# Kernel optimization log

Measured on AMD Instinct MI355X. Metric: run time of the kernel, lower is better.

The kernel has to match this reference:

```python
import jax, jax.numpy as jnp
import numpy as np

N, C, B = 131072, 256, 2
Z, Y, X = 32, 240, 240  # spconv coord order: batch, z, y, x
EPS = 1e-5


def _build_sparse():
    """Generate unique sparse voxel coords and per-axis 3-tap submanifold
    neighbor tables (rulebook). Sentinel index N marks a missing neighbor."""
    rng = np.random.default_rng(0)
    per = N // B
    coords = []
    for b in range(B):
        lin = rng.choice(Z * Y * X, per, replace=False)
        z, r = np.divmod(lin, Y * X)
        y, x = np.divmod(r, X)
        coords.append(np.stack([np.full(per, b), z, y, x], 1))
    coords = np.concatenate(coords, 0).astype(np.int64)
    keys = ((coords[:, 0] * Z + coords[:, 1]) * Y + coords[:, 2]) * X + coords[:, 3]
    order = np.argsort(keys)
    coords, keys = coords[order], keys[order]

    def nbr_axis(axis, bound):
        out = np.full((N, 3), N, dtype=np.int64)
        for k, off in enumerate((-1, 0, 1)):
            c = coords.copy()
            c[:, axis] += off
            valid = (c[:, axis] >= 0) & (c[:, axis] < bound)
            qk = ((c[:, 0] * Z + c[:, 1]) * Y + c[:, 2]) * X + c[:, 3]
            pos = np.clip(np.searchsorted(keys, qk), 0, N - 1)
            hit = valid & (keys[pos] == qk)
            out[:, k] = np.where(hit, pos, N)
        return out

    return nbr_axis(1, Z), nbr_axis(2, Y), nbr_axis(3, X)


def setup_inputs() -> dict:
    nbr1, nbr2, nbr3 = _build_sparse()
    key = jax.random.key(0)
    ks = jax.random.split(key, 4)
    scale = 0.02  # keep pre-sigmoid activations in a sane range
    return {
        "features": jax.random.normal(ks[0], (N, C), jnp.float32),
        "W1": jax.random.normal(ks[1], (3, C, C), jnp.float32) * scale,
        "W2": jax.random.normal(ks[2], (3, C, C), jnp.float32) * scale,
        "W3": jax.random.normal(ks[3], (3, C, C), jnp.float32) * scale,
        "g1": jnp.ones((C,), jnp.float32), "b1": jnp.zeros((C,), jnp.float32),
        "g2": jnp.ones((C,), jnp.float32), "b2": jnp.zeros((C,), jnp.float32),
        "g3": jnp.ones((C,), jnp.float32), "b3": jnp.zeros((C,), jnp.float32),
        "nbr1": jnp.asarray(nbr1), "nbr2": jnp.asarray(nbr2), "nbr3": jnp.asarray(nbr3),
    }


def _subm_conv(fp, nbr, W):
    # fp: [N+1, C] (last row zero pad), nbr: [N, 3], W: [3, Cin, Cout]
    return fp[nbr[:, 0]] @ W[0] + fp[nbr[:, 1]] @ W[1] + fp[nbr[:, 2]] @ W[2]


def _bn(h, g, b):
    mu = h.mean(0)
    var = h.var(0)  # biased, matches torch BN normalization in train mode
    return g * (h - mu) * jax.lax.rsqrt(var + EPS) + b


def reference(features, W1, W2, W3, g1, b1, g2, b2, g3, b3, nbr1, nbr2, nbr3):
    pad = jnp.zeros((1, features.shape[1]), features.dtype)
    fp = jnp.concatenate([features, pad], 0)  # [N+1, C]
    s1 = jax.nn.sigmoid(_bn(_subm_conv(fp, nbr1, W1), g1, b1))
    s2 = jax.nn.sigmoid(_bn(_subm_conv(fp, nbr2, W2), g2, b2))
    s3 = jax.nn.sigmoid(_bn(_subm_conv(fp, nbr3, W3), g3, b3))
    return (s1 + s2 + s3) * features
```

## Files before the change

kernel.cpp:

```cpp
#include <hip/hip_runtime.h>
#include <hip/hip_bf16.h>


#define NP 131072
#define CC 256

typedef __attribute__((ext_vector_type(4))) float f32x4;
typedef __attribute__((ext_vector_type(8))) short bf16x8;

__device__ __forceinline__ unsigned short f2bf(float f) {
    unsigned int u = __float_as_uint(f);
    u += 0x7FFFu + ((u >> 16) & 1u);
    return (unsigned short)(u >> 16);
}
__device__ __forceinline__ float bf2f(unsigned short s) {
    return __uint_as_float(((unsigned int)s) << 16);
}

__device__ __forceinline__ void gload_lds16(const void* g, void* l) {
    __builtin_amdgcn_global_load_lds(
        (const __attribute__((address_space(1))) unsigned int*)g,
        (__attribute__((address_space(3))) unsigned int*)l, 16, 0, 0);
}

__global__ void zero_stats_k(float* stats) {
    int i = blockIdx.x * 256 + threadIdx.x;
    if (i < 3 * 2 * CC) stats[i] = 0.f;
}

__global__ void cast_features_k(const float* __restrict__ f, unsigned short* __restrict__ fb) {
    size_t e = ((size_t)blockIdx.x * 256 + threadIdx.x) * 8;
    const size_t tot = (size_t)(NP + 1) * CC;
    if (e >= tot) return;
    unsigned short tmp[8];
    if (e >= (size_t)NP * CC) {
        #pragma unroll
        for (int j = 0; j < 8; ++j) tmp[j] = 0;
    } else {
        float4 v0 = *(const float4*)(f + e);
        float4 v1 = *(const float4*)(f + e + 4);
        tmp[0] = f2bf(v0.x); tmp[1] = f2bf(v0.y); tmp[2] = f2bf(v0.z); tmp[3] = f2bf(v0.w);
        tmp[4] = f2bf(v1.x); tmp[5] = f2bf(v1.y); tmp[6] = f2bf(v1.z); tmp[7] = f2bf(v1.w);
    }
    *(bf16x8*)(fb + e) = *(bf16x8*)tmp;
}

__global__ void cast_weights_k(const float* __restrict__ W1, const float* __restrict__ W2,
                               const float* __restrict__ W3, unsigned short* __restrict__ wbT) {
    int bid  = blockIdx.x;
    int m    = bid >> 8;
    int cout = bid & 255;
    int cin  = threadIdx.x;
    const float* W = (m < 3) ? W1 : (m < 6) ? W2 : W3;
    int tap = m - (m / 3) * 3;
    float v = W[((size_t)tap * CC + cin) * CC + cout];
    wbT[((size_t)m * CC + cout) * CC + cin] = f2bf(v);
}

__global__ __launch_bounds__(256)
void gemm_conv_fused_k(const unsigned short* __restrict__ fb,
                       const unsigned short* __restrict__ wbT,
                       const int* __restrict__ nbr1, const int* __restrict__ nbr2,
                       const int* __restrict__ nbr3,
                       unsigned short* __restrict__ hbase,
                       float* __restrict__ statsBase) {
    __shared__ unsigned short As[128 * 32];
    __shared__ unsigned short Bs[128 * 32];
    __shared__ int rowIdx[3 * 128];
    __shared__ float colsum[128];
    __shared__ float colsq[128];

    const int axis = blockIdx.z;
    const int* nbr = (axis == 0) ? nbr1 : (axis == 1) ? nbr2 : nbr3;
    const unsigned short* wT = wbT + (size_t)axis * 3 * CC * CC;
    unsigned short* h = hbase + (size_t)axis * NP * CC;
    float* stats = statsBase + axis * 2 * CC;

    const int tid     = threadIdx.x;
    const int lane    = tid & 63;
    const int wave    = tid >> 6;
    const int colBase = blockIdx.x * 128;
    const int rowBase = blockIdx.y * 128;

    if (tid < 128) {
        int i = rowBase + tid;
        rowIdx[tid]       = nbr[(size_t)i * 3 + 0];
        rowIdx[128 + tid] = nbr[(size_t)i * 3 + 1];
        rowIdx[256 + tid] = nbr[(size_t)i * 3 + 2];
        colsum[tid] = 0.f;
        colsq[tid]  = 0.f;
    }

    f32x4 acc[4][4] = {};

    const int wr     = wave >> 1;
    const int wc     = wave & 1;
    const int fr     = lane & 15;
    const int sSub   = lane >> 2;
    const int sChunk = lane & 3;
    const int gChunk = sChunk ^ ((sSub >> 1) & 3);
    const int rChunkOff = ((lane >> 4) ^ ((fr >> 1) & 3)) * 8;

    __syncthreads();

    for (int tap = 0; tap < 3; ++tap) {
        const unsigned short* wTt = wT + (size_t)tap * CC * CC;
        const int* rIdx = rowIdx + tap * 128;
        for (int kk = 0; kk < CC; kk += 32) {
            #pragma unroll
            for (int u = 0; u < 2; ++u) {
                int q  = wave * 2 + u;
                int ar = rIdx[q * 16 + sSub];
                const unsigned short* asrc = fb + ((size_t)ar * CC + kk + gChunk * 8);
                gload_lds16(asrc, As + q * 512);
                int bc = colBase + q * 16 + sSub;
                const unsigned short* bsrc = wTt + ((size_t)bc * CC + kk + gChunk * 8);
                gload_lds16(bsrc, Bs + q * 512);
            }
            __syncthreads();

            bf16x8 aF[4], bF[4];
            #pragma unroll
            for (int m = 0; m < 4; ++m)
                aF[m] = *(const bf16x8*)(As + (wr * 64 + m * 16 + fr) * 32 + rChunkOff);
            #pragma unroll
            for (int n = 0; n < 4; ++n)
                bF[n] = *(const bf16x8*)(Bs + (wc * 64 + n * 16 + fr) * 32 + rChunkOff);
            #pragma unroll
            for (int m = 0; m < 4; ++m)
                #pragma unroll
                for (int n = 0; n < 4; ++n)
                    acc[m][n] = __builtin_amdgcn_mfma_f32_16x16x32_bf16(aF[m], bF[n], acc[m][n], 0, 0, 0);
            __syncthreads();
        }
    }

    const int orow = (lane >> 4) * 4;
    float psum[4], psq[4];
    #pragma unroll
    for (int n = 0; n < 4; ++n) { psum[n] = 0.f; psq[n] = 0.f; }
    #pragma unroll
    for (int m = 0; m < 4; ++m) {
        #pragma unroll
        for (int n = 0; n < 4; ++n) {
            int col = colBase + wc * 64 + n * 16 + fr;
            int row = rowBase + wr * 64 + m * 16 + orow;
            #pragma unroll
            for (int j = 0; j < 4; ++j) {
                unsigned short hb = f2bf(acc[m][n][j]);
                float v = bf2f(hb);
                h[(size_t)(row + j) * CC + col] = hb;
                psum[n] += v;
                psq[n]  += v * v;
            }
        }
    }
    #pragma unroll
    for (int n = 0; n < 4; ++n) {
        psum[n] += __shfl_xor(psum[n], 16);
        psum[n] += __shfl_xor(psum[n], 32);
        psq[n]  += __shfl_xor(psq[n], 16);
        psq[n]  += __shfl_xor(psq[n], 32);
    }
    if ((lane >> 4) == 0) {
        #pragma unroll
        for (int n = 0; n < 4; ++n) {
            int cl = wc * 64 + n * 16 + fr;
            atomicAdd(&colsum[cl], psum[n]);
            atomicAdd(&colsq[cl],  psq[n]);
        }
    }
    __syncthreads();
    if (tid < 128) {
        int c = colBase + tid;
        atomicAdd(&stats[c],      colsum[tid]);
        atomicAdd(&stats[CC + c], colsq[tid]);
    }
}

__global__ void finalize3_k(const float* __restrict__ stats,
                            const float* __restrict__ g1, const float* __restrict__ b1,
                            const float* __restrict__ g2, const float* __restrict__ b2,
                            const float* __restrict__ g3, const float* __restrict__ b3,
                            float* __restrict__ ss) {
    int a = blockIdx.x;
    int c = threadIdx.x;
    const float* g = (a == 0) ? g1 : (a == 1) ? g2 : g3;
    const float* b = (a == 0) ? b1 : (a == 1) ? b2 : b3;
    const float* st = stats + a * 2 * CC;
    float* s = ss + a * 2 * CC;
    float mu  = st[c] * (1.f / NP);
    float var = st[CC + c] * (1.f / NP) - mu * mu;
    float sc  = g[c] * rsqrtf(var + 1e-5f);
    s[c]      = sc;
    s[CC + c] = b[c] - mu * sc;
}

__global__ void apply3_k(const unsigned short* __restrict__ h1,
                         const unsigned short* __restrict__ h2,
                         const unsigned short* __restrict__ h3,
                         const float* __restrict__ ss,
                         const float* __restrict__ feat, float* __restrict__ out) {
    size_t e = ((size_t)blockIdx.x * 256 + threadIdx.x) * 8;
    int c0 = (int)(e & (CC - 1));
    bf16x8 v1 = *(const bf16x8*)(h1 + e);
    bf16x8 v2 = *(const bf16x8*)(h2 + e);
    bf16x8 v3 = *(const bf16x8*)(h3 + e);
    float s[8];
    #pragma unroll
    for (int j = 0; j < 8; ++j) {
        float z1 = ss[c0 + j]            * bf2f((unsigned short)v1[j]) + ss[CC + c0 + j];
        float z2 = ss[2 * CC + c0 + j]   * bf2f((unsigned short)v2[j]) + ss[3 * CC + c0 + j];
        float z3 = ss[4 * CC + c0 + j]   * bf2f((unsigned short)v3[j]) + ss[5 * CC + c0 + j];
        s[j] = 1.f / (1.f + __expf(-z1)) + 1.f / (1.f + __expf(-z2)) + 1.f / (1.f + __expf(-z3));
    }
    const float4* fv = (const float4*)(feat + e);
    float4 f0 = fv[0], f1 = fv[1];
    float4* o = (float4*)(out + e);
    o[0] = make_float4(s[0] * f0.x, s[1] * f0.y, s[2] * f0.z, s[3] * f0.w);
    o[1] = make_float4(s[4] * f1.x, s[5] * f1.y, s[6] * f1.z, s[7] * f1.w);
}

extern "C" void kernel_launch(void* const* d_in, const int* in_sizes, int n_in,
                              void* d_out, int out_size, void* d_ws, size_t ws_size,
                              hipStream_t stream) {
    const float* feat = (const float*)d_in[0];
    const float* W1   = (const float*)d_in[1];
    const float* W2   = (const float*)d_in[2];
    const float* W3   = (const float*)d_in[3];
    const float* g1   = (const float*)d_in[4];
    const float* b1   = (const float*)d_in[5];
    const float* g2   = (const float*)d_in[6];
    const float* b2   = (const float*)d_in[7];
    const float* g3   = (const float*)d_in[8];
    const float* b3   = (const float*)d_in[9];
    const int* nbr1   = (const int*)d_in[10];
    const int* nbr2   = (const int*)d_in[11];
    const int* nbr3   = (const int*)d_in[12];
    float* out = (float*)d_out;

    char* w = (char*)d_ws;
    unsigned short* fb   = (unsigned short*)w;  w += (size_t)(NP + 1) * CC * 2;
    unsigned short* wbT  = (unsigned short*)w;  w += (size_t)9 * CC * CC * 2;
    float* stats         = (float*)w;           w += (size_t)3 * 2 * CC * 4;
    float* ss            = (float*)w;           w += (size_t)3 * 2 * CC * 4;
    unsigned short* hbuf = (unsigned short*)w;

    zero_stats_k<<<6, 256, 0, stream>>>(stats);
    {
        size_t tot = (size_t)(NP + 1) * CC / 8;
        int blocks = (int)((tot + 255) / 256);
        cast_features_k<<<blocks, 256, 0, stream>>>(feat, fb);
    }
    cast_weights_k<<<2304, 256, 0, stream>>>(W1, W2, W3, wbT);

    gemm_conv_fused_k<<<dim3(2, 1024, 3), 256, 0, stream>>>(fb, wbT, nbr1, nbr2, nbr3,
                                                            hbuf, stats);
    finalize3_k<<<3, 256, 0, stream>>>(stats, g1, b1, g2, b2, g3, b3, ss);
    apply3_k<<<16384, 256, 0, stream>>>(hbuf,
                                        hbuf + (size_t)NP * CC,
                                        hbuf + (size_t)2 * NP * CC,
                                        ss, feat, out);
}
```

Baseline: 321.8 us.

## Rewrite gathered conv GEMM with 256x256 tiles and double-buffered LDS pipeline

The conv GEMM is restructured so each 512-thread block computes a 256-row by full 256-column tile with BK=64. LDS is double-buffered, and the async global-to-LDS loads for the next k-step are interleaved with MFMA phases, using setprio and barriers to overlap memory and compute. Each gathered feature row is now read once instead of once per column half, which cuts gather traffic. The epilogue and apply kernel use nontemporal loads and stores, and the apply kernel reads bf16 features instead of fp32. That last change introduces rounding error in the final multiply by the features.

```diff
diff --git a/kernel.cpp b/kernel.cpp
--- a/kernel.cpp
+++ b/kernel.cpp
@@ -4,6 +4,10 @@
 
 #define NP 131072
 #define CC 256
+#define BM 256
+#define BK 64
+#define ATILE (BM * BK)
+#define BTILE (256 * BK)
 
 typedef __attribute__((ext_vector_type(4))) float f32x4;
 typedef __attribute__((ext_vector_type(8))) short bf16x8;
@@ -57,82 +61,155 @@
     wbT[((size_t)m * CC + cout) * CC + cin] = f2bf(v);
 }
 
-__global__ __launch_bounds__(256)
+#define MFMA16(a, b, c) __builtin_amdgcn_mfma_f32_16x16x32_bf16((a), (b), (c), 0, 0, 0)
+#define LDF(base, row, swz) (*(const bf16x8*)((base) + (row) * BK + (swz)))
+
+__global__ __launch_bounds__(512, 2)
 void gemm_conv_fused_k(const unsigned short* __restrict__ fb,
                        const unsigned short* __restrict__ wbT,
                        const int* __restrict__ nbr1, const int* __restrict__ nbr2,
                        const int* __restrict__ nbr3,
                        unsigned short* __restrict__ hbase,
                        float* __restrict__ statsBase) {
-    __shared__ unsigned short As[128 * 32];
-    __shared__ unsigned short Bs[128 * 32];
-    __shared__ int rowIdx[3 * 128];
-    __shared__ float colsum[128];
-    __shared__ float colsq[128];
-
-    const int axis = blockIdx.z;
+    __shared__ unsigned short As[2 * ATILE];
+    __shared__ unsigned short Bs[2 * BTILE];
+    __shared__ float colsum[256];
+    __shared__ float colsq[256];
+
+    const int axis = blockIdx.y;
     const int* nbr = (axis == 0) ? nbr1 : (axis == 1) ? nbr2 : nbr3;
-    const unsigned short* wT = wbT + (size_t)axis * 3 * CC * CC;
+    const unsigned short* wA = wbT + (size_t)axis * 3 * CC * CC;
     unsigned short* h = hbase + (size_t)axis * NP * CC;
     float* stats = statsBase + axis * 2 * CC;
 
     const int tid     = threadIdx.x;
     const int lane    = tid & 63;
     const int wave    = tid >> 6;
-    const int colBase = blockIdx.x * 128;
-    const int rowBase = blockIdx.y * 128;
-
-    if (tid < 128) {
-        int i = rowBase + tid;
-        rowIdx[tid]       = nbr[(size_t)i * 3 + 0];
-        rowIdx[128 + tid] = nbr[(size_t)i * 3 + 1];
-        rowIdx[256 + tid] = nbr[(size_t)i * 3 + 2];
-        colsum[tid] = 0.f;
-        colsq[tid]  = 0.f;
-    }
-
-    f32x4 acc[4][4] = {};
-
-    const int wr     = wave >> 1;
-    const int wc     = wave & 1;
-    const int fr     = lane & 15;
-    const int sSub   = lane >> 2;
-    const int sChunk = lane & 3;
-    const int gChunk = sChunk ^ ((sSub >> 1) & 3);
-    const int rChunkOff = ((lane >> 4) ^ ((fr >> 1) & 3)) * 8;
-
+    const int rowBase = blockIdx.x * BM;
+
+    if (tid < 256) { colsum[tid] = 0.f; colsq[tid] = 0.f; }
+
+    int rstage[4], srcOff[4];
+    int gA0[4], gA1[4], gA2[4];
+    #pragma unroll
+    for (int u = 0; u < 4; ++u) {
+        int idx = u * 512 + tid;
+        int r = idx >> 3, p = idx & 7;
+        rstage[u] = r;
+        srcOff[u] = (p ^ (r & 7)) * 8;
+        int gi = rowBase + r;
+        gA0[u] = nbr[(size_t)gi * 3 + 0];
+        gA1[u] = nbr[(size_t)gi * 3 + 1];
+        gA2[u] = nbr[(size_t)gi * 3 + 2];
+    }
+
+#define STAGE_A(u, Abuf, tapsel, kkE) do {                                    \
+        int gr_ = ((tapsel) == 0) ? gA0[u] : ((tapsel) == 1) ? gA1[u] : gA2[u]; \
+        gload_lds16(fb + (size_t)gr_ * CC + (kkE) + srcOff[u],                \
+                    (Abuf) + ((u) * 512 + wave * 64) * 8);                    \
+    } while (0)
+#define STAGE_B(u, Bbuf, wTt, kkE)                                            \
+        gload_lds16((wTt) + (size_t)rstage[u] * CC + (kkE) + srcOff[u],       \
+                    (Bbuf) + ((u) * 512 + wave * 64) * 8)
+
+    const int wr = wave >> 2;
+    const int wc = wave & 3;
+    const int fr = lane & 15;
+    const int kq = lane >> 4;
+    const int swz0 = (kq ^ (fr & 7)) * 8;
+    const int swz1 = ((4 + kq) ^ (fr & 7)) * 8;
+    const int rA = wr * 128 + fr;
+    const int rB = wc * 64 + fr;
+
+    f32x4 acc[8][4] = {};
+
+    STAGE_A(0, As, 0, 0); STAGE_A(1, As, 0, 0); STAGE_A(2, As, 0, 0); STAGE_A(3, As, 0, 0);
+    STAGE_B(0, Bs, wA, 0); STAGE_B(1, Bs, wA, 0); STAGE_B(2, Bs, wA, 0); STAGE_B(3, Bs, wA, 0);
     __syncthreads();
 
-    for (int tap = 0; tap < 3; ++tap) {
-        const unsigned short* wTt = wT + (size_t)tap * CC * CC;
-        const int* rIdx = rowIdx + tap * 128;
-        for (int kk = 0; kk < CC; kk += 32) {
-            #pragma unroll
-            for (int u = 0; u < 2; ++u) {
-                int q  = wave * 2 + u;
-                int ar = rIdx[q * 16 + sSub];
-                const unsigned short* asrc = fb + ((size_t)ar * CC + kk + gChunk * 8);
-                gload_lds16(asrc, As + q * 512);
-                int bc = colBase + q * 16 + sSub;
-                const unsigned short* bsrc = wTt + ((size_t)bc * CC + kk + gChunk * 8);
-                gload_lds16(bsrc, Bs + q * 512);
-            }
-            __syncthreads();
-
-            bf16x8 aF[4], bF[4];
-            #pragma unroll
-            for (int m = 0; m < 4; ++m)
-                aF[m] = *(const bf16x8*)(As + (wr * 64 + m * 16 + fr) * 32 + rChunkOff);
-            #pragma unroll
-            for (int n = 0; n < 4; ++n)
-                bF[n] = *(const bf16x8*)(Bs + (wc * 64 + n * 16 + fr) * 32 + rChunkOff);
-            #pragma unroll
-            for (int m = 0; m < 4; ++m)
-                #pragma unroll
-                for (int n = 0; n < 4; ++n)
-                    acc[m][n] = __builtin_amdgcn_mfma_f32_16x16x32_bf16(aF[m], bF[n], acc[m][n], 0, 0, 0);
-            __syncthreads();
-        }
+    for (int t = 0; t < 12; ++t) {
+        unsigned short* Ac = As + (t & 1) * ATILE;
+        unsigned short* Bc = Bs + (t & 1) * BTILE;
+        unsigned short* An = As + ((t & 1) ^ 1) * ATILE;
+        unsigned short* Bn = Bs + ((t & 1) ^ 1) * BTILE;
+        const int t1 = t + 1;
+        const int tap1 = t1 >> 2;
+        const int kk1 = (t1 & 3) * BK;
+        const unsigned short* wT1 = wA + (size_t)tap1 * CC * CC;
+        const bool st = (t < 11);
+
+        bf16x8 aF[4][2], bLo[2][2], bHi[2][2];
+
+        #pragma unroll
+        for (int m = 0; m < 4; ++m) {
+            aF[m][0] = LDF(Ac, rA + m * 16, swz0);
+            aF[m][1] = LDF(Ac, rA + m * 16, swz1);
+        }
+        #pragma unroll
+        for (int n = 0; n < 2; ++n) {
+            bLo[n][0] = LDF(Bc, rB + n * 16, swz0);
+            bLo[n][1] = LDF(Bc, rB + n * 16, swz1);
+        }
+        if (st) { STAGE_A(0, An, tap1, kk1); STAGE_A(1, An, tap1, kk1); STAGE_B(0, Bn, wT1, kk1); }
+        __builtin_amdgcn_s_barrier();
+        __builtin_amdgcn_s_setprio(1);
+        #pragma unroll
+        for (int m = 0; m < 4; ++m)
+            #pragma unroll
+            for (int n = 0; n < 2; ++n) {
+                acc[m][n] = MFMA16(aF[m][0], bLo[n][0], acc[m][n]);
+                acc[m][n] = MFMA16(aF[m][1], bLo[n][1], acc[m][n]);
+            }
+        __builtin_amdgcn_s_setprio(0);
+        __builtin_amdgcn_s_barrier();
+
+        #pragma unroll
+        for (int n = 0; n < 2; ++n) {
+            bHi[n][0] = LDF(Bc, rB + (n + 2) * 16, swz0);
+            bHi[n][1] = LDF(Bc, rB + (n + 2) * 16, swz1);
+        }
+        if (st) { STAGE_A(2, An, tap1, kk1); STAGE_A(3, An, tap1, kk1); STAGE_B(1, Bn, wT1, kk1); }
+        __builtin_amdgcn_s_barrier();
+        __builtin_amdgcn_s_setprio(1);
+        #pragma unroll
+        for (int m = 0; m < 4; ++m)
+            #pragma unroll
+            for (int n = 0; n < 2; ++n) {
+                acc[m][n + 2] = MFMA16(aF[m][0], bHi[n][0], acc[m][n + 2]);
+                acc[m][n + 2] = MFMA16(aF[m][1], bHi[n][1], acc[m][n + 2]);
+            }
+        __builtin_amdgcn_s_setprio(0);
+        __builtin_amdgcn_s_barrier();
+
+        #pragma unroll
+        for (int m = 0; m < 4; ++m) {
+            aF[m][0] = LDF(Ac, rA + (m + 4) * 16, swz0);
+            aF[m][1] = LDF(Ac, rA + (m + 4) * 16, swz1);
+        }
+        if (st) { STAGE_B(2, Bn, wT1, kk1); STAGE_B(3, Bn, wT1, kk1); }
+        __builtin_amdgcn_s_barrier();
+        __builtin_amdgcn_s_setprio(1);
+        #pragma unroll
+        for (int m = 0; m < 4; ++m)
+            #pragma unroll
+            for (int n = 0; n < 2; ++n) {
+                acc[m + 4][n + 2] = MFMA16(aF[m][0], bHi[n][0], acc[m + 4][n + 2]);
+                acc[m + 4][n + 2] = MFMA16(aF[m][1], bHi[n][1], acc[m + 4][n + 2]);
+            }
+        __builtin_amdgcn_s_setprio(0);
+        __builtin_amdgcn_s_barrier();
+
+        __builtin_amdgcn_s_setprio(1);
+        #pragma unroll
+        for (int m = 0; m < 4; ++m)
+            #pragma unroll
+            for (int n = 0; n < 2; ++n) {
+                acc[m + 4][n] = MFMA16(aF[m][0], bLo[n][0], acc[m + 4][n]);
+                acc[m + 4][n] = MFMA16(aF[m][1], bLo[n][1], acc[m + 4][n]);
+            }
+        __builtin_amdgcn_s_setprio(0);
+        if (st) asm volatile("s_waitcnt vmcnt(0)" ::: "memory");
+        __builtin_amdgcn_s_barrier();
     }
 
     const int orow = (lane >> 4) * 4;
@@ -140,16 +217,16 @@
     #pragma unroll
     for (int n = 0; n < 4; ++n) { psum[n] = 0.f; psq[n] = 0.f; }
     #pragma unroll
-    for (int m = 0; m < 4; ++m) {
+    for (int m = 0; m < 8; ++m) {
         #pragma unroll
         for (int n = 0; n < 4; ++n) {
-            int col = colBase + wc * 64 + n * 16 + fr;
-            int row = rowBase + wr * 64 + m * 16 + orow;
+            int col = wc * 64 + n * 16 + fr;
+            int row = rowBase + wr * 128 + m * 16 + orow;
             #pragma unroll
             for (int j = 0; j < 4; ++j) {
                 unsigned short hb = f2bf(acc[m][n][j]);
                 float v = bf2f(hb);
-                h[(size_t)(row + j) * CC + col] = hb;
+                __builtin_nontemporal_store(hb, &h[(size_t)(row + j) * CC + col]);
                 psum[n] += v;
                 psq[n]  += v * v;
             }
@@ -171,11 +248,12 @@
         }
     }
     __syncthreads();
-    if (tid < 128) {
-        int c = colBase + tid;
-        atomicAdd(&stats[c],      colsum[tid]);
-        atomicAdd(&stats[CC + c], colsq[tid]);
-    }
+    if (tid < 256) {
+        atomicAdd(&stats[tid],      colsum[tid]);
+        atomicAdd(&stats[CC + tid], colsq[tid]);
+    }
+#undef STAGE_A
+#undef STAGE_B
 }
 
 __global__ void finalize3_k(const float* __restrict__ stats,
@@ -200,25 +278,27 @@
                          const unsigned short* __restrict__ h2,
                          const unsigned short* __restrict__ h3,
                          const float* __restrict__ ss,
-                         const float* __restrict__ feat, float* __restrict__ out) {
+                         const unsigned short* __restrict__ fb, float* __restrict__ out) {
     size_t e = ((size_t)blockIdx.x * 256 + threadIdx.x) * 8;
     int c0 = (int)(e & (CC - 1));
-    bf16x8 v1 = *(const bf16x8*)(h1 + e);
-    bf16x8 v2 = *(const bf16x8*)(h2 + e);
-    bf16x8 v3 = *(const bf16x8*)(h3 + e);
+    bf16x8 v1 = __builtin_nontemporal_load((const bf16x8*)(h1 + e));
+    bf16x8 v2 = __builtin_nontemporal_load((const bf16x8*)(h2 + e));
+    bf16x8 v3 = __builtin_nontemporal_load((const bf16x8*)(h3 + e));
+    bf16x8 fv = *(const bf16x8*)(fb + e);
     float s[8];
     #pragma unroll
     for (int j = 0; j < 8; ++j) {
-        float z1 = ss[c0 + j]            * bf2f((unsigned short)v1[j]) + ss[CC + c0 + j];
-        float z2 = ss[2 * CC + c0 + j]   * bf2f((unsigned short)v2[j]) + ss[3 * CC + c0 + j];
-        float z3 = ss[4 * CC + c0 + j]   * bf2f((unsigned short)v3[j]) + ss[5 * CC + c0 + j];
-        s[j] = 1.f / (1.f + __expf(-z1)) + 1.f / (1.f + __expf(-z2)) + 1.f / (1.f + __expf(-z3));
-    }
-    const float4* fv = (const float4*)(feat + e);
-    float4 f0 = fv[0], f1 = fv[1];
-    float4* o = (float4*)(out + e);
-    o[0] = make_float4(s[0] * f0.x, s[1] * f0.y, s[2] * f0.z, s[3] * f0.w);
-    o[1] = make_float4(s[4] * f1.x, s[5] * f1.y, s[6] * f1.z, s[7] * f1.w);
+        float z1 = ss[c0 + j]          * bf2f((unsigned short)v1[j]) + ss[CC + c0 + j];
+        float z2 = ss[2 * CC + c0 + j] * bf2f((unsigned short)v2[j]) + ss[3 * CC + c0 + j];
+        float z3 = ss[4 * CC + c0 + j] * bf2f((unsigned short)v3[j]) + ss[5 * CC + c0 + j];
+        float sg = 1.f / (1.f + __expf(-z1)) + 1.f / (1.f + __expf(-z2)) + 1.f / (1.f + __expf(-z3));
+        s[j] = sg * bf2f((unsigned short)fv[j]);
+    }
+    f32x4* o = (f32x4*)(out + e);
+    f32x4 o0 = {s[0], s[1], s[2], s[3]};
+    f32x4 o1 = {s[4], s[5], s[6], s[7]};
+    __builtin_nontemporal_store(o0, o);
+    __builtin_nontemporal_store(o1, o + 1);
 }
 
 extern "C" void kernel_launch(void* const* d_in, const int* in_sizes, int n_in,
@@ -254,11 +334,11 @@
     }
     cast_weights_k<<<2304, 256, 0, stream>>>(W1, W2, W3, wbT);
 
-    gemm_conv_fused_k<<<dim3(2, 1024, 3), 256, 0, stream>>>(fb, wbT, nbr1, nbr2, nbr3,
-                                                            hbuf, stats);
+    gemm_conv_fused_k<<<dim3(512, 3), 512, 0, stream>>>(fb, wbT, nbr1, nbr2, nbr3,
+                                                        hbuf, stats);
     finalize3_k<<<3, 256, 0, stream>>>(stats, g1, b1, g2, b2, g3, b3, ss);
     apply3_k<<<16384, 256, 0, stream>>>(hbuf,
                                         hbuf + (size_t)NP * CC,
                                         hbuf + (size_t)2 * NP * CC,
-                                        ss, feat, out);
-}
+                                        ss, fb, out);
+}
```

Result: slower. 405.6 us (+26.0%).

## Double-buffer the gather-GEMM LDS tiles and read bf16 features in apply

Applied to the files above, without the earlier changes.

The conv GEMM now double-buffers its A and B LDS tiles over a flattened 24-step tap/K loop. The loads for the next step are issued before the MFMAs of the current one, leaving one barrier per step. Neighbor indices stay in registers, blocks are swizzled over a 2D grid, and launch bounds request 3 blocks per CU. The apply kernel reads the bf16 copy of the features instead of fp32 and uses nontemporal loads and stores to cut traffic, at the cost of bf16 rounding in the final multiply.

```diff
diff --git a/kernel.cpp b/kernel.cpp
--- a/kernel.cpp
+++ b/kernel.cpp
@@ -4,6 +4,7 @@
 
 #define NP 131072
 #define CC 256
+#define TILEE (128 * 32)
 
 typedef __attribute__((ext_vector_type(4))) float f32x4;
 typedef __attribute__((ext_vector_type(8))) short bf16x8;
@@ -57,82 +58,101 @@
     wbT[((size_t)m * CC + cout) * CC + cin] = f2bf(v);
 }
 
-__global__ __launch_bounds__(256)
+#define MFMA16(a, b, c) __builtin_amdgcn_mfma_f32_16x16x32_bf16((a), (b), (c), 0, 0, 0)
+
+__global__ __launch_bounds__(256, 3)
 void gemm_conv_fused_k(const unsigned short* __restrict__ fb,
                        const unsigned short* __restrict__ wbT,
                        const int* __restrict__ nbr1, const int* __restrict__ nbr2,
                        const int* __restrict__ nbr3,
                        unsigned short* __restrict__ hbase,
                        float* __restrict__ statsBase) {
-    __shared__ unsigned short As[128 * 32];
-    __shared__ unsigned short Bs[128 * 32];
-    __shared__ int rowIdx[3 * 128];
+    __shared__ unsigned short As[2][TILEE];
+    __shared__ unsigned short Bs[2][TILEE];
     __shared__ float colsum[128];
     __shared__ float colsq[128];
 
-    const int axis = blockIdx.z;
+    const int axis = blockIdx.y;
     const int* nbr = (axis == 0) ? nbr1 : (axis == 1) ? nbr2 : nbr3;
-    const unsigned short* wT = wbT + (size_t)axis * 3 * CC * CC;
+    const unsigned short* wA = wbT + (size_t)axis * 3 * CC * CC;
     unsigned short* h = hbase + (size_t)axis * NP * CC;
     float* stats = statsBase + axis * 2 * CC;
 
-    const int tid     = threadIdx.x;
-    const int lane    = tid & 63;
-    const int wave    = tid >> 6;
-    const int colBase = blockIdx.x * 128;
-    const int rowBase = blockIdx.y * 128;
-
-    if (tid < 128) {
-        int i = rowBase + tid;
-        rowIdx[tid]       = nbr[(size_t)i * 3 + 0];
-        rowIdx[128 + tid] = nbr[(size_t)i * 3 + 1];
-        rowIdx[256 + tid] = nbr[(size_t)i * 3 + 2];
-        colsum[tid] = 0.f;
-        colsq[tid]  = 0.f;
-    }
+    const int tid  = threadIdx.x;
+    const int lane = tid & 63;
+    const int wave = tid >> 6;
+    const int bx   = blockIdx.x;
+    const int swzb = (bx & 7) * 256 + (bx >> 3);
+    const int rowBase = (swzb >> 1) * 128;
+    const int colBase = (swzb & 1) * 128;
+
+    if (tid < 128) { colsum[tid] = 0.f; colsq[tid] = 0.f; }
+
+    int srcOff[2], gA0[2], gA1[2], gA2[2], bRow[2];
+    #pragma unroll
+    for (int u = 0; u < 2; ++u) {
+        int idx = u * 256 + tid;
+        int r = idx >> 2, p = idx & 3;
+        srcOff[u] = (p ^ ((r >> 1) & 3)) * 8;
+        int gi = rowBase + r;
+        gA0[u] = nbr[(size_t)gi * 3 + 0];
+        gA1[u] = nbr[(size_t)gi * 3 + 1];
+        gA2[u] = nbr[(size_t)gi * 3 + 2];
+        bRow[u] = colBase + r;
+    }
+
+#define STAGE_A(u, Abuf, tapsel, kkE) do {                                      \
+        int gr_ = ((tapsel) == 0) ? gA0[u] : ((tapsel) == 1) ? gA1[u] : gA2[u]; \
+        gload_lds16(fb + (size_t)gr_ * CC + (kkE) + srcOff[u],                  \
+                    (Abuf) + ((u) * 256 + tid) * 8);                            \
+    } while (0)
+#define STAGE_B(u, Bbuf, wTt, kkE)                                              \
+        gload_lds16((wTt) + (size_t)bRow[u] * CC + (kkE) + srcOff[u],           \
+                    (Bbuf) + ((u) * 256 + tid) * 8)
+
+    const int wr = (wave >> 1) & 1;
+    const int wc = wave & 1;
+    const int fr = lane & 15;
+    const int kq = lane >> 4;
+    const int chunkOff = (kq ^ ((fr >> 1) & 3)) * 8;
+    const int rA = wr * 64 + fr;
+    const int rB = wc * 64 + fr;
 
     f32x4 acc[4][4] = {};
 
-    const int wr     = wave >> 1;
-    const int wc     = wave & 1;
-    const int fr     = lane & 15;
-    const int sSub   = lane >> 2;
-    const int sChunk = lane & 3;
-    const int gChunk = sChunk ^ ((sSub >> 1) & 3);
-    const int rChunkOff = ((lane >> 4) ^ ((fr >> 1) & 3)) * 8;
-
+    STAGE_A(0, As[0], 0, 0); STAGE_A(1, As[0], 0, 0);
+    STAGE_B(0, Bs[0], wA, 0); STAGE_B(1, Bs[0], wA, 0);
     __syncthreads();
 
-    for (int tap = 0; tap < 3; ++tap) {
-        const unsigned short* wTt = wT + (size_t)tap * CC * CC;
-        const int* rIdx = rowIdx + tap * 128;
-        for (int kk = 0; kk < CC; kk += 32) {
-            #pragma unroll
-            for (int u = 0; u < 2; ++u) {
-                int q  = wave * 2 + u;
-                int ar = rIdx[q * 16 + sSub];
-                const unsigned short* asrc = fb + ((size_t)ar * CC + kk + gChunk * 8);
-                gload_lds16(asrc, As + q * 512);
-                int bc = colBase + q * 16 + sSub;
-                const unsigned short* bsrc = wTt + ((size_t)bc * CC + kk + gChunk * 8);
-                gload_lds16(bsrc, Bs + q * 512);
-            }
-            __syncthreads();
-
-            bf16x8 aF[4], bF[4];
-            #pragma unroll
-            for (int m = 0; m < 4; ++m)
-                aF[m] = *(const bf16x8*)(As + (wr * 64 + m * 16 + fr) * 32 + rChunkOff);
+    for (int t = 0; t < 24; ++t) {
+        const unsigned short* Ac = As[t & 1];
+        const unsigned short* Bc = Bs[t & 1];
+        unsigned short* An = As[(t + 1) & 1];
+        unsigned short* Bn = Bs[(t + 1) & 1];
+        const int t1 = t + 1;
+        const int tap1 = t1 >> 3;
+        const int kk1 = (t1 & 7) * 32;
+
+        if (t < 23) {
+            const unsigned short* wT1 = wA + (size_t)tap1 * CC * CC;
+            STAGE_A(0, An, tap1, kk1); STAGE_A(1, An, tap1, kk1);
+            STAGE_B(0, Bn, wT1, kk1);  STAGE_B(1, Bn, wT1, kk1);
+        }
+
+        bf16x8 aF[4], bF[4];
+        #pragma unroll
+        for (int m = 0; m < 4; ++m)
+            aF[m] = *(const bf16x8*)(Ac + (rA + m * 16) * 32 + chunkOff);
+        #pragma unroll
+        for (int n = 0; n < 4; ++n)
+            bF[n] = *(const bf16x8*)(Bc + (rB + n * 16) * 32 + chunkOff);
+        #pragma unroll
+        for (int m = 0; m < 4; ++m)
             #pragma unroll
             for (int n = 0; n < 4; ++n)
-                bF[n] = *(const bf16x8*)(Bs + (wc * 64 + n * 16 + fr) * 32 + rChunkOff);
-            #pragma unroll
-            for (int m = 0; m < 4; ++m)
-                #pragma unroll
-                for (int n = 0; n < 4; ++n)
-                    acc[m][n] = __builtin_amdgcn_mfma_f32_16x16x32_bf16(aF[m], bF[n], acc[m][n], 0, 0, 0);
-            __syncthreads();
-        }
+                acc[m][n] = MFMA16(aF[m], bF[n], acc[m][n]);
+
+        __syncthreads();
     }
 
     const int orow = (lane >> 4) * 4;
@@ -176,6 +196,8 @@
         atomicAdd(&stats[c],      colsum[tid]);
         atomicAdd(&stats[CC + c], colsq[tid]);
     }
+#undef STAGE_A
+#undef STAGE_B
 }
 
 __global__ void finalize3_k(const float* __restrict__ stats,
@@ -200,25 +222,27 @@
                          const unsigned short* __restrict__ h2,
                          const unsigned short* __restrict__ h3,
                          const float* __restrict__ ss,
-                         const float* __restrict__ feat, float* __restrict__ out) {
+                         const unsigned short* __restrict__ fb, float* __restrict__ out) {
     size_t e = ((size_t)blockIdx.x * 256 + threadIdx.x) * 8;
     int c0 = (int)(e & (CC - 1));
-    bf16x8 v1 = *(const bf16x8*)(h1 + e);
-    bf16x8 v2 = *(const bf16x8*)(h2 + e);
-    bf16x8 v3 = *(const bf16x8*)(h3 + e);
+    bf16x8 v1 = __builtin_nontemporal_load((const bf16x8*)(h1 + e));
+    bf16x8 v2 = __builtin_nontemporal_load((const bf16x8*)(h2 + e));
+    bf16x8 v3 = __builtin_nontemporal_load((const bf16x8*)(h3 + e));
+    bf16x8 fv = *(const bf16x8*)(fb + e);
     float s[8];
     #pragma unroll
     for (int j = 0; j < 8; ++j) {
-        float z1 = ss[c0 + j]            * bf2f((unsigned short)v1[j]) + ss[CC + c0 + j];
-        float z2 = ss[2 * CC + c0 + j]   * bf2f((unsigned short)v2[j]) + ss[3 * CC + c0 + j];
-        float z3 = ss[4 * CC + c0 + j]   * bf2f((unsigned short)v3[j]) + ss[5 * CC + c0 + j];
-        s[j] = 1.f / (1.f + __expf(-z1)) + 1.f / (1.f + __expf(-z2)) + 1.f / (1.f + __expf(-z3));
-    }
-    const float4* fv = (const float4*)(feat + e);
-    float4 f0 = fv[0], f1 = fv[1];
-    float4* o = (float4*)(out + e);
-    o[0] = make_float4(s[0] * f0.x, s[1] * f0.y, s[2] * f0.z, s[3] * f0.w);
-    o[1] = make_float4(s[4] * f1.x, s[5] * f1.y, s[6] * f1.z, s[7] * f1.w);
+        float z1 = ss[c0 + j]          * bf2f((unsigned short)v1[j]) + ss[CC + c0 + j];
+        float z2 = ss[2 * CC + c0 + j] * bf2f((unsigned short)v2[j]) + ss[3 * CC + c0 + j];
+        float z3 = ss[4 * CC + c0 + j] * bf2f((unsigned short)v3[j]) + ss[5 * CC + c0 + j];
+        float sg = 1.f / (1.f + __expf(-z1)) + 1.f / (1.f + __expf(-z2)) + 1.f / (1.f + __expf(-z3));
+        s[j] = sg * bf2f((unsigned short)fv[j]);
+    }
+    f32x4* o = (f32x4*)(out + e);
+    f32x4 o0 = {s[0], s[1], s[2], s[3]};
+    f32x4 o1 = {s[4], s[5], s[6], s[7]};
+    __builtin_nontemporal_store(o0, o);
+    __builtin_nontemporal_store(o1, o + 1);
 }
 
 extern "C" void kernel_launch(void* const* d_in, const int* in_sizes, int n_in,
@@ -254,11 +278,11 @@
     }
     cast_weights_k<<<2304, 256, 0, stream>>>(W1, W2, W3, wbT);
 
-    gemm_conv_fused_k<<<dim3(2, 1024, 3), 256, 0, stream>>>(fb, wbT, nbr1, nbr2, nbr3,
-                                                            hbuf, stats);
+    gemm_conv_fused_k<<<dim3(2048, 3), 256, 0, stream>>>(fb, wbT, nbr1, nbr2, nbr3,
+                                                         hbuf, stats);
     finalize3_k<<<3, 256, 0, stream>>>(stats, g1, b1, g2, b2, g3, b3, ss);
     apply3_k<<<16384, 256, 0, stream>>>(hbuf,
                                         hbuf + (size_t)NP * CC,
                                         hbuf + (size_t)2 * NP * CC,
-                                        ss, feat, out);
-}
+                                        ss, fb, out);
+}
```

Measured after the change: 276.5 us. 14.1% less time.
